# Optimization experiments

Measured on AMD Instinct MI355X. Metric: run time of the kernel, lower is better.

The kernel has to match this reference:

```python
import jax, jax.numpy as jnp
import numpy as np

# Sizes (see init_kwargs / shape_source)
N = 65536      # total points
B = 8          # batch elements
PPB = N // B   # points per batch element (8192, divisible by WS -> no padding)
D = 256        # d_model
H = 8          # nhead
DH = D // H
L = 4          # num_layers
FF = 2048      # torch TransformerEncoderLayer default dim_feedforward
RES = 128      # resolution (coordinate range / embedding table size)
BITS = 7       # ceil(log2(RES)); higher bits of morton loop are zero
WS = 128       # window_size
EPS = 1e-5     # LayerNorm eps


def setup_inputs() -> dict:
    key = jax.random.key(0)
    ks = jax.random.split(key, 16)
    s = 0.02
    batch_col = (jnp.arange(N) // PPB).astype(jnp.int32)
    xyz = jax.random.randint(ks[0], (N, 3), 0, RES, dtype=jnp.int32)
    coords = jnp.concatenate([batch_col[:, None], xyz], axis=1)
    features = jax.random.normal(ks[1], (N, D), jnp.float32)
    inp = {
        'coords': coords,
        'features': features,
        # learned positional embedding tables
        'pe_x': jax.random.normal(ks[2], (RES, D), jnp.float32) * s,
        'pe_y': jax.random.normal(ks[3], (RES, D), jnp.float32) * s,
        'pe_z': jax.random.normal(ks[4], (RES, D), jnp.float32) * s,
        'pe_s': jax.random.normal(ks[5], (RES, D), jnp.float32) * s,
        # stacked transformer encoder layer params (torch post-norm layer)
        'Wqkv': jax.random.normal(ks[6], (L, 3 * D, D), jnp.float32) * s,
        'bqkv': jnp.zeros((L, 3 * D), jnp.float32),
        'Wo': jax.random.normal(ks[7], (L, D, D), jnp.float32) * s,
        'bo': jnp.zeros((L, D), jnp.float32),
        'W1': jax.random.normal(ks[8], (L, FF, D), jnp.float32) * s,
        'b1': jnp.zeros((L, FF), jnp.float32),
        'W2': jax.random.normal(ks[9], (L, D, FF), jnp.float32) * s,
        'b2': jnp.zeros((L, D), jnp.float32),
        'g1': jnp.ones((L, D), jnp.float32),
        'be1': jnp.zeros((L, D), jnp.float32),
        'g2': jnp.ones((L, D), jnp.float32),
        'be2': jnp.zeros((L, D), jnp.float32),
    }
    return inp


def _morton_key(coords):
    # interleave bits of x,y,z (z lowest), prefix with batch index so batch order is preserved
    x, y, z = coords[:, 1], coords[:, 2], coords[:, 3]
    m = jnp.zeros_like(x)
    for i in range(BITS):
        m = m | (((x >> i) & 1) << (3 * i + 2)) \
              | (((y >> i) & 1) << (3 * i + 1)) \
              | (((z >> i) & 1) << (3 * i))
    return coords[:, 0] * (1 << (3 * BITS)) + m


def _ln(x, g, b):
    mu = jnp.mean(x, axis=-1, keepdims=True)
    var = jnp.mean(jnp.square(x - mu), axis=-1, keepdims=True)
    return (x - mu) * jax.lax.rsqrt(var + EPS) * g + b


def _encoder(x, params):
    # x: [Wn, WS, D]; torch TransformerEncoderLayer, post-norm, relu, no dropout (eval)
    scale = float(DH) ** -0.5

    def layer(h, p):
        Wqkv, bqkv, Wo, bo, W1, b1, W2, b2, g1, be1, g2, be2 = p
        Wn = h.shape[0]
        qkv = h @ Wqkv.T + bqkv                      # [Wn, WS, 3D]
        q, k, v = jnp.split(qkv, 3, axis=-1)
        q = q.reshape(Wn, WS, H, DH)
        k = k.reshape(Wn, WS, H, DH)
        v = v.reshape(Wn, WS, H, DH)
        att = jax.nn.softmax(jnp.einsum('wqhd,wkhd->whqk', q, k) * scale, axis=-1)
        o = jnp.einsum('whqk,wkhd->wqhd', att, v).reshape(Wn, WS, D) @ Wo.T + bo
        h = _ln(h + o, g1, be1)
        ff = jax.nn.relu(h @ W1.T + b1) @ W2.T + b2
        h = _ln(h + ff, g2, be2)
        return h, None

    x, _ = jax.lax.scan(layer, x, params)
    return x


def reference(coords, features, pe_x, pe_y, pe_z, pe_s,
              Wqkv, bqkv, Wo, bo, W1, b1, W2, b2, g1, be1, g2, be2):
    # 1) Morton sort (stable, batch-major)
    idx = jnp.argsort(_morton_key(coords))
    sc = coords[idx]
    sf = features[idx]
    # 2) learned positional encoding (stride = 1)
    pe = pe_x[sc[:, 1]] + pe_y[sc[:, 2]] + pe_z[sc[:, 3]] + pe_s[1]
    x = sf + pe
    # 3) window split: PPB % WS == 0, interval == 1 -> exact tiling, no padding
    x = x.reshape(-1, WS, D)                          # [Wn, WS, D]
    # 4) transformer encoder over windows
    x = _encoder(x, (Wqkv, bqkv, Wo, bo, W1, b1, W2, b2, g1, be1, g2, be2))
    # 5) gather back (all masks True -> simple reshape); output in sorted order
    return x.reshape(N, D)
```

## Files before the change

### kernel.cpp

```cpp
#include <hip/hip_runtime.h>

typedef unsigned int u32;
typedef unsigned short u16;

#define NPTS 65536
#define DMODEL 256
#define NHEAD 8
#define DHEAD 32
#define NLAYER 4
#define FFDIM 2048
#define WSIZE 128
#define LNEPS 1e-5f
#define RG 256

#define KSTR 36
#define VSTR 132
#define PSTR 132

typedef __attribute__((ext_vector_type(8))) short short8;
typedef __attribute__((ext_vector_type(4))) float floatx4;

__device__ __forceinline__ float bf2f(u16 v) {
    u32 u = ((u32)v) << 16;
    float f;
    __builtin_memcpy(&f, &u, 4);
    return f;
}
__device__ __forceinline__ u16 f2bf(float f) {
    u32 u;
    __builtin_memcpy(&u, &f, 4);
    u32 r = (u + 0x7fffu + ((u >> 16) & 1u)) >> 16;
    return (u16)r;
}

__device__ __forceinline__ void gl_lds16(const void* g, void* l) {
    __builtin_amdgcn_global_load_lds((const __attribute__((address_space(1))) u32*)g,
                                     (__attribute__((address_space(3))) u32*)l, 16, 0, 0);
}

__global__ __launch_bounds__(256) void morton_kernel(const int* __restrict__ coords,
                                                     u32* __restrict__ key, u32* __restrict__ val) {
    int i = blockIdx.x * 256 + threadIdx.x;
    int b = coords[4 * i + 0];
    int x = coords[4 * i + 1];
    int y = coords[4 * i + 2];
    int z = coords[4 * i + 3];
    u32 m = 0;
#pragma unroll
    for (int t = 0; t < 7; ++t) {
        m |= ((u32)((x >> t) & 1) << (3 * t + 2)) | ((u32)((y >> t) & 1) << (3 * t + 1)) |
             ((u32)((z >> t) & 1) << (3 * t));
    }
    key[i] = ((u32)b << 21) | m;
    val[i] = (u32)i;
}

__global__ __launch_bounds__(256) void hist_kernel(const u32* __restrict__ key, u32* __restrict__ ghist,
                                                   int shift) {
    __shared__ u32 h[256];
    int tid = threadIdx.x;
    h[tid] = 0;
    __syncthreads();
    u32 k = key[blockIdx.x * 256 + tid];
    atomicAdd(&h[(k >> shift) & 255u], 1u);
    __syncthreads();
    ghist[(size_t)tid * RG + blockIdx.x] = h[tid];
}

__global__ __launch_bounds__(256) void scan_up(u32* __restrict__ g, u32* __restrict__ aux) {
    __shared__ u32 wsum[4];
    int tid = threadIdx.x;
    int lane = tid & 63;
    int wave = tid >> 6;
    size_t base = (size_t)blockIdx.x * 1024 + (size_t)tid * 4;
    uint4 v = *(const uint4*)(g + base);
    u32 s = v.x + v.y + v.z + v.w;
    u32 inc = s;
#pragma unroll
    for (int off = 1; off < 64; off <<= 1) {
        u32 u = __shfl_up(inc, off, 64);
        if (lane >= off) inc += u;
    }
    if (lane == 63) wsum[wave] = inc;
    __syncthreads();
    u32 woff = 0;
    for (int w = 0; w < wave; ++w) woff += wsum[w];
    u32 excl = woff + inc - s;
    uint4 o;
    o.x = excl;
    o.y = excl + v.x;
    o.z = excl + v.x + v.y;
    o.w = excl + v.x + v.y + v.z;
    *(uint4*)(g + base) = o;
    if (tid == 255) aux[blockIdx.x] = woff + inc;
}

__global__ __launch_bounds__(256) void scan_down(u32* __restrict__ g, const u32* __restrict__ aux) {
    __shared__ u32 boff;
    int tid = threadIdx.x;
    if (tid < 64) {
        u32 a = (tid < (int)blockIdx.x) ? aux[tid] : 0u;
#pragma unroll
        for (int off = 32; off > 0; off >>= 1) a += __shfl_xor(a, off, 64);
        if (tid == 0) boff = a;
    }
    __syncthreads();
    u32 s = boff;
    size_t base = (size_t)blockIdx.x * 1024 + (size_t)tid * 4;
    uint4 v = *(uint4*)(g + base);
    v.x += s;
    v.y += s;
    v.z += s;
    v.w += s;
    *(uint4*)(g + base) = v;
}

__global__ __launch_bounds__(256) void scatter_kernel(const u32* __restrict__ keyin, const u32* __restrict__ valin,
                                                      u32* __restrict__ keyout, u32* __restrict__ valout,
                                                      const u32* __restrict__ ghist, int shift) {
    __shared__ u32 whist[4][256];
    int tid = threadIdx.x;
    int lane = tid & 63;
    int wave = tid >> 6;
    uint4 z = {0u, 0u, 0u, 0u};
    ((uint4*)&whist[0][0])[tid] = z;
    int gi = blockIdx.x * 256 + tid;
    u32 k = keyin[gi];
    u32 v = valin[gi];
    u32 b = (k >> shift) & 255u;
    __syncthreads();
    unsigned long long m = ~0ull;
#pragma unroll
    for (int bit = 0; bit < 8; ++bit) {
        unsigned long long bb = __ballot((int)((b >> bit) & 1u));
        m &= ((b >> bit) & 1u) ? bb : ~bb;
    }
    unsigned long long below = (lane == 0) ? 0ull : (m & ((1ull << lane) - 1ull));
    int rlane = __popcll(below);
    int cnt = __popcll(m);
    if (rlane == 0) whist[wave][b] = (u32)cnt;
    __syncthreads();
    u32 rank = (u32)rlane;
    for (int w = 0; w < wave; ++w) rank += whist[w][b];
    u32 dst = ghist[(size_t)b * RG + blockIdx.x] + rank;
    keyout[dst] = k;
    valout[dst] = v;
}

__global__ __launch_bounds__(256) void cvt_bf16_kernel(const float* __restrict__ in, u16* __restrict__ out, int n) {
    int i = blockIdx.x * 256 + threadIdx.x;
    if (i < n) out[i] = f2bf(in[i]);
}

template <bool HF32>
__global__ __launch_bounds__(256) void gather_pe_kernel(const u32* __restrict__ idx, const int* __restrict__ coords,
                                                        const float* __restrict__ feat,
                                                        const float* __restrict__ pex, const float* __restrict__ pey,
                                                        const float* __restrict__ pez, const float* __restrict__ pes,
                                                        float* __restrict__ h, u16* __restrict__ xb) {
    int row = blockIdx.x * 4 + (threadIdx.x >> 6);
    int lane = threadIdx.x & 63;
    int src = (int)idx[row];
    int cx = coords[4 * src + 1];
    int cy = coords[4 * src + 2];
    int cz = coords[4 * src + 3];
    int c = lane * 4;
    float4 f = *(const float4*)(feat + (size_t)src * DMODEL + c);
    float4 px = *(const float4*)(pex + (size_t)cx * DMODEL + c);
    float4 py = *(const float4*)(pey + (size_t)cy * DMODEL + c);
    float4 pz = *(const float4*)(pez + (size_t)cz * DMODEL + c);
    float4 ps = *(const float4*)(pes + (size_t)1 * DMODEL + c);
    float4 r;
    r.x = f.x + px.x + py.x + pz.x + ps.x;
    r.y = f.y + px.y + py.y + pz.y + ps.y;
    r.z = f.z + px.z + py.z + pz.z + ps.z;
    r.w = f.w + px.w + py.w + pz.w + ps.w;
    if (HF32) *(float4*)(h + (size_t)row * DMODEL + c) = r;
    ushort4 o;
    o.x = f2bf(r.x);
    o.y = f2bf(r.y);
    o.z = f2bf(r.z);
    o.w = f2bf(r.w);
    *(ushort4*)(xb + (size_t)row * DMODEL + c) = o;
}

template <bool RELU, bool BF16OUT>
__global__ __launch_bounds__(256) void gemm_bt(const u16* __restrict__ A, const u16* __restrict__ W,
                                               const float* __restrict__ bias, void* __restrict__ Cout,
                                               int M, int O, int K) {
    __shared__ __align__(16) u16 lA[128 * 64];
    __shared__ __align__(16) u16 lB[128 * 64];
    const int tid = threadIdx.x;
    const int lane = tid & 63;
    const int wave = tid >> 6;
    const int wr = wave >> 1;
    const int wc = wave & 1;
    const int quad = lane >> 4;
    const int l16 = lane & 15;
    const size_t row0 = (size_t)blockIdx.x * 128;
    const size_t col0 = (size_t)blockIdx.y * 128;
    floatx4 acc[4][4] = {};
    const u16* Abase = A + row0 * (size_t)K;
    const u16* Wbase = W + col0 * (size_t)K;

    for (int k0 = 0; k0 < K; k0 += 64) {
        __syncthreads();
#pragma unroll
        for (int it = 0; it < 4; ++it) {
            int cidx = tid + it * 256;
            int r = cidx >> 3;
            int cc = (cidx & 7) << 3;
            gl_lds16(Abase + (size_t)r * K + k0 + cc, &lA[cidx * 8]);
            gl_lds16(Wbase + (size_t)r * K + k0 + cc, &lB[cidx * 8]);
        }
        __syncthreads();
#pragma unroll
        for (int kk = 0; kk < 64; kk += 32) {
            short8 af[4], bf[4];
#pragma unroll
            for (int r = 0; r < 4; ++r)
                af[r] = *(const short8*)&lA[(wr * 64 + r * 16 + l16) * 64 + kk + quad * 8];
#pragma unroll
            for (int c = 0; c < 4; ++c)
                bf[c] = *(const short8*)&lB[(wc * 64 + c * 16 + l16) * 64 + kk + quad * 8];
#pragma unroll
            for (int r = 0; r < 4; ++r)
#pragma unroll
                for (int c = 0; c < 4; ++c)
                    acc[r][c] = __builtin_amdgcn_mfma_f32_16x16x32_bf16(af[r], bf[c], acc[r][c], 0, 0, 0);
        }
    }

#pragma unroll
    for (int r = 0; r < 4; ++r) {
#pragma unroll
        for (int c = 0; c < 4; ++c) {
            size_t col = col0 + wc * 64 + c * 16 + l16;
            float bv = bias[col];
#pragma unroll
            for (int reg = 0; reg < 4; ++reg) {
                size_t row = row0 + wr * 64 + r * 16 + quad * 4 + reg;
                float v = acc[r][c][reg] + bv;
                if (RELU) v = fmaxf(v, 0.f);
                if (BF16OUT)
                    ((u16*)Cout)[row * O + col] = f2bf(v);
                else
                    ((float*)Cout)[row * O + col] = v;
            }
        }
    }
}

__global__ __launch_bounds__(128) void attn_kernel(const u16* __restrict__ qkv, u16* __restrict__ outb) {
    const int wh = blockIdx.x;
    const int w = wh >> 3;
    const int h = wh & 7;
    const int tid = threadIdx.x;
    const int wave = tid >> 6;
    const int lane = tid & 63;
    const int quad = lane >> 4;
    const int l16 = lane & 15;
    __shared__ __align__(16) u16 lK[128 * KSTR];
    __shared__ __align__(16) u16 lVt[32 * VSTR];
    __shared__ __align__(16) u16 lP[128 * PSTR];
    const u16* base = qkv + (size_t)w * WSIZE * (3 * DMODEL);

    {
        const u16* krow = base + (size_t)tid * (3 * DMODEL) + DMODEL + h * DHEAD;
        const u16* vrow = base + (size_t)tid * (3 * DMODEL) + 2 * DMODEL + h * DHEAD;
#pragma unroll
        for (int p = 0; p < 4; ++p)
            *(short8*)&lK[tid * KSTR + p * 8] = *(const short8*)(krow + p * 8);
        u16 varr[32];
#pragma unroll
        for (int p = 0; p < 4; ++p)
            *(short8*)&varr[p * 8] = *(const short8*)(vrow + p * 8);
#pragma unroll
        for (int d = 0; d < DHEAD; ++d) lVt[d * VSTR + tid] = varr[d];
    }
    short8 af[4];
#pragma unroll
    for (int mi = 0; mi < 4; ++mi)
        af[mi] = *(const short8*)(base + (size_t)(wave * 64 + mi * 16 + l16) * (3 * DMODEL) + h * DHEAD + quad * 8);
    __syncthreads();

    floatx4 acc[4][8] = {};
#pragma unroll
    for (int ni = 0; ni < 8; ++ni) {
        short8 bk = *(const short8*)&lK[(ni * 16 + l16) * KSTR + quad * 8];
#pragma unroll
        for (int mi = 0; mi < 4; ++mi)
            acc[mi][ni] = __builtin_amdgcn_mfma_f32_16x16x32_bf16(af[mi], bk, acc[mi][ni], 0, 0, 0);
    }

    const float scale = 0.17677669529663687f;
    float inv[4][4];
#pragma unroll
    for (int mi = 0; mi < 4; ++mi) {
#pragma unroll
        for (int reg = 0; reg < 4; ++reg) {
            float m = acc[mi][0][reg];
#pragma unroll
            for (int ni = 1; ni < 8; ++ni) m = fmaxf(m, acc[mi][ni][reg]);
            m = fmaxf(m, __shfl_xor(m, 1, 64));
            m = fmaxf(m, __shfl_xor(m, 2, 64));
            m = fmaxf(m, __shfl_xor(m, 4, 64));
            m = fmaxf(m, __shfl_xor(m, 8, 64));
            float e[8];
            float sum = 0.f;
#pragma unroll
            for (int ni = 0; ni < 8; ++ni) {
                e[ni] = __expf((acc[mi][ni][reg] - m) * scale);
                sum += e[ni];
            }
            sum += __shfl_xor(sum, 1, 64);
            sum += __shfl_xor(sum, 2, 64);
            sum += __shfl_xor(sum, 4, 64);
            sum += __shfl_xor(sum, 8, 64);
            inv[mi][reg] = 1.f / sum;
            int row = wave * 64 + mi * 16 + quad * 4 + reg;
#pragma unroll
            for (int ni = 0; ni < 8; ++ni) lP[row * PSTR + ni * 16 + l16] = f2bf(e[ni]);
        }
    }

    floatx4 acc2[4][2] = {};
#pragma unroll
    for (int kt = 0; kt < 4; ++kt) {
        short8 pa[4];
#pragma unroll
        for (int mi = 0; mi < 4; ++mi)
            pa[mi] = *(const short8*)&lP[(wave * 64 + mi * 16 + l16) * PSTR + kt * 32 + quad * 8];
#pragma unroll
        for (int c = 0; c < 2; ++c) {
            short8 bv = *(const short8*)&lVt[(c * 16 + l16) * VSTR + kt * 32 + quad * 8];
#pragma unroll
            for (int mi = 0; mi < 4; ++mi)
                acc2[mi][c] = __builtin_amdgcn_mfma_f32_16x16x32_bf16(pa[mi], bv, acc2[mi][c], 0, 0, 0);
        }
    }

#pragma unroll
    for (int mi = 0; mi < 4; ++mi) {
#pragma unroll
        for (int c = 0; c < 2; ++c) {
#pragma unroll
            for (int reg = 0; reg < 4; ++reg) {
                int row = wave * 64 + mi * 16 + quad * 4 + reg;
                outb[(size_t)(w * WSIZE + row) * DMODEL + h * DHEAD + c * 16 + l16] =
                    f2bf(acc2[mi][c][reg] * inv[mi][reg]);
            }
        }
    }
}

template <bool HF32, bool OUTF32>
__global__ __launch_bounds__(256) void resid_ln_kernel(const void* __restrict__ hin, const float* __restrict__ delta,
                                                       const float* __restrict__ g, const float* __restrict__ b,
                                                       float* __restrict__ hout, void* __restrict__ nout) {
    int row = blockIdx.x * 4 + (threadIdx.x >> 6);
    int lane = threadIdx.x & 63;
    int c = lane * 4;
    float4 x;
    if (HF32) {
        x = *(const float4*)((const float*)hin + (size_t)row * DMODEL + c);
    } else {
        ushort4 hv = *(const ushort4*)((const u16*)hin + (size_t)row * DMODEL + c);
        x.x = bf2f(hv.x);
        x.y = bf2f(hv.y);
        x.z = bf2f(hv.z);
        x.w = bf2f(hv.w);
    }
    float4 d = *(const float4*)(delta + (size_t)row * DMODEL + c);
    x.x += d.x;
    x.y += d.y;
    x.z += d.z;
    x.w += d.w;
    float s = x.x + x.y + x.z + x.w;
#pragma unroll
    for (int off = 32; off > 0; off >>= 1) s += __shfl_xor(s, off, 64);
    float mu = s * (1.f / 256.f);
    float d0 = x.x - mu, d1 = x.y - mu, d2 = x.z - mu, d3 = x.w - mu;
    float vs = d0 * d0 + d1 * d1 + d2 * d2 + d3 * d3;
#pragma unroll
    for (int off = 32; off > 0; off >>= 1) vs += __shfl_xor(vs, off, 64);
    float rs = rsqrtf(vs * (1.f / 256.f) + LNEPS);
    float4 gg = *(const float4*)(g + c);
    float4 bb = *(const float4*)(b + c);
    float4 y;
    y.x = d0 * rs * gg.x + bb.x;
    y.y = d1 * rs * gg.y + bb.y;
    y.z = d2 * rs * gg.z + bb.z;
    y.w = d3 * rs * gg.w + bb.w;
    if (HF32) *(float4*)(hout + (size_t)row * DMODEL + c) = y;
    if (OUTF32) {
        *(float4*)((float*)nout + (size_t)row * DMODEL + c) = y;
    } else {
        ushort4 o;
        o.x = f2bf(y.x);
        o.y = f2bf(y.y);
        o.z = f2bf(y.z);
        o.w = f2bf(y.w);
        *(ushort4*)((u16*)nout + (size_t)row * DMODEL + c) = o;
    }
}

extern "C" void kernel_launch(void* const* d_in, const int* in_sizes, int n_in,
                              void* d_out, int out_size, void* d_ws, size_t ws_size,
                              hipStream_t stream) {
    (void)in_sizes;
    (void)n_in;
    (void)out_size;
    const int* coords = (const int*)d_in[0];
    const float* feat = (const float*)d_in[1];
    const float* pex = (const float*)d_in[2];
    const float* pey = (const float*)d_in[3];
    const float* pez = (const float*)d_in[4];
    const float* pes = (const float*)d_in[5];
    const float* Wqkv = (const float*)d_in[6];
    const float* bqkv = (const float*)d_in[7];
    const float* Wo = (const float*)d_in[8];
    const float* bo = (const float*)d_in[9];
    const float* W1 = (const float*)d_in[10];
    const float* b1 = (const float*)d_in[11];
    const float* W2 = (const float*)d_in[12];
    const float* b2 = (const float*)d_in[13];
    const float* g1 = (const float*)d_in[14];
    const float* be1 = (const float*)d_in[15];
    const float* g2 = (const float*)d_in[16];
    const float* be2 = (const float*)d_in[17];

    auto al = [](size_t x) { return (x + 255) & ~(size_t)255; };
    const size_t sortB = 4 * al((size_t)NPTS * 4) + al((size_t)256 * RG * 4) + 256;
    const size_t wqkvB = al((size_t)NLAYER * 3 * DMODEL * DMODEL * 2);
    const size_t woB = al((size_t)NLAYER * DMODEL * DMODEL * 2);
    const size_t w1B = al((size_t)NLAYER * FFDIM * DMODEL * 2);
    const size_t w2B = al((size_t)NLAYER * DMODEL * FFDIM * 2);
    const size_t wB = wqkvB + woB + w1B + w2B;
    const size_t xbB = al((size_t)NPTS * DMODEL * 2);
    const size_t hB = al((size_t)NPTS * DMODEL * 4);

    int CH = 0;
    bool modeA = true;
    for (int ch = 16384; ch >= 128; ch >>= 1) {
        size_t need = sortB + wB + xbB + hB + al((size_t)ch * 4096) + al((size_t)ch * 1024) + 65536;
        if (need <= ws_size) { CH = ch; modeA = true; break; }
    }
    if (!CH) {
        for (int ch = 16384; ch >= 128; ch >>= 1) {
            size_t need = sortB + wB + xbB + al((size_t)ch * 4096) + al((size_t)ch * 1024) + 65536;
            if (need <= ws_size) { CH = ch; modeA = false; break; }
        }
    }
    if (!CH) { CH = 128; modeA = false; }

    char* ws = (char*)d_ws;
    size_t off = 0;
    auto alloc = [&](size_t bytes) -> void* {
        void* p = ws + off;
        off += al(bytes);
        return p;
    };
    u32* key0 = (u32*)alloc(NPTS * 4);
    u32* val0 = (u32*)alloc(NPTS * 4);
    u32* key1 = (u32*)alloc(NPTS * 4);
    u32* val1 = (u32*)alloc(NPTS * 4);
    u32* ghist = (u32*)alloc(256 * RG * 4);
    u32* aux = (u32*)alloc(64 * 4);
    u16* wqkv_b = (u16*)alloc((size_t)NLAYER * 3 * DMODEL * DMODEL * 2);
    u16* wo_b = (u16*)alloc((size_t)NLAYER * DMODEL * DMODEL * 2);
    u16* w1_b = (u16*)alloc((size_t)NLAYER * FFDIM * DMODEL * 2);
    u16* w2_b = (u16*)alloc((size_t)NLAYER * DMODEL * FFDIM * 2);
    u16* xb = (u16*)alloc((size_t)NPTS * DMODEL * 2);
    float* h = modeA ? (float*)alloc((size_t)NPTS * DMODEL * 4) : nullptr;
    u16* scratch1 = (u16*)alloc((size_t)CH * 4096);
    float* tmpc = (float*)alloc((size_t)CH * 1024);

    morton_kernel<<<NPTS / 256, 256, 0, stream>>>(coords, key0, val0);

    u32 *ki = key0, *vi = val0, *ko = key1, *vo = val1;
    for (int p = 0; p < 3; ++p) {
        hist_kernel<<<RG, 256, 0, stream>>>(ki, ghist, p * 8);
        scan_up<<<64, 256, 0, stream>>>(ghist, aux);
        scan_down<<<64, 256, 0, stream>>>(ghist, aux);
        scatter_kernel<<<RG, 256, 0, stream>>>(ki, vi, ko, vo, ghist, p * 8);
        u32* t;
        t = ki; ki = ko; ko = t;
        t = vi; vi = vo; vo = t;
    }
    const u32* idx = vi;

    cvt_bf16_kernel<<<(NLAYER * 3 * DMODEL * DMODEL) / 256, 256, 0, stream>>>(Wqkv, wqkv_b, NLAYER * 3 * DMODEL * DMODEL);
    cvt_bf16_kernel<<<(NLAYER * DMODEL * DMODEL) / 256, 256, 0, stream>>>(Wo, wo_b, NLAYER * DMODEL * DMODEL);
    cvt_bf16_kernel<<<(NLAYER * FFDIM * DMODEL) / 256, 256, 0, stream>>>(W1, w1_b, NLAYER * FFDIM * DMODEL);
    cvt_bf16_kernel<<<(NLAYER * DMODEL * FFDIM) / 256, 256, 0, stream>>>(W2, w2_b, NLAYER * DMODEL * FFDIM);

    if (modeA)
        gather_pe_kernel<true><<<NPTS / 4, 256, 0, stream>>>(idx, coords, feat, pex, pey, pez, pes, h, xb);
    else
        gather_pe_kernel<false><<<NPTS / 4, 256, 0, stream>>>(idx, coords, feat, pex, pey, pez, pes, nullptr, xb);

    const int nch = NPTS / CH;
    u16* qkvc = scratch1;
    u16* attoutc = scratch1 + (size_t)CH * 768;
    u16* midc = scratch1;
    for (int l = 0; l < NLAYER; ++l) {
        for (int c = 0; c < nch; ++c) {
            u16* xc = xb + (size_t)c * CH * DMODEL;
            float* hc = modeA ? h + (size_t)c * CH * DMODEL : nullptr;
            gemm_bt<false, true><<<dim3(CH / 128, (3 * DMODEL) / 128), 256, 0, stream>>>(
                xc, wqkv_b + (size_t)l * 3 * DMODEL * DMODEL, bqkv + (size_t)l * 3 * DMODEL, qkvc,
                CH, 3 * DMODEL, DMODEL);
            attn_kernel<<<(CH / WSIZE) * NHEAD, 128, 0, stream>>>(qkvc, attoutc);
            gemm_bt<false, false><<<dim3(CH / 128, DMODEL / 128), 256, 0, stream>>>(
                attoutc, wo_b + (size_t)l * DMODEL * DMODEL, bo + (size_t)l * DMODEL, tmpc,
                CH, DMODEL, DMODEL);
            if (modeA)
                resid_ln_kernel<true, false><<<CH / 4, 256, 0, stream>>>(hc, tmpc, g1 + (size_t)l * DMODEL,
                                                                         be1 + (size_t)l * DMODEL, hc, xc);
            else
                resid_ln_kernel<false, false><<<CH / 4, 256, 0, stream>>>(xc, tmpc, g1 + (size_t)l * DMODEL,
                                                                          be1 + (size_t)l * DMODEL, nullptr, xc);
            gemm_bt<true, true><<<dim3(CH / 128, FFDIM / 128), 256, 0, stream>>>(
                xc, w1_b + (size_t)l * FFDIM * DMODEL, b1 + (size_t)l * FFDIM, midc,
                CH, FFDIM, DMODEL);
            gemm_bt<false, false><<<dim3(CH / 128, DMODEL / 128), 256, 0, stream>>>(
                midc, w2_b + (size_t)l * DMODEL * FFDIM, b2 + (size_t)l * DMODEL, tmpc,
                CH, DMODEL, FFDIM);
            bool last = (l == NLAYER - 1);
            void* outc = last ? (void*)((float*)d_out + (size_t)c * CH * DMODEL) : (void*)xc;
            if (modeA) {
                if (last)
                    resid_ln_kernel<true, true><<<CH / 4, 256, 0, stream>>>(hc, tmpc, g2 + (size_t)l * DMODEL,
                                                                            be2 + (size_t)l * DMODEL, hc, outc);
                else
                    resid_ln_kernel<true, false><<<CH / 4, 256, 0, stream>>>(hc, tmpc, g2 + (size_t)l * DMODEL,
                                                                             be2 + (size_t)l * DMODEL, hc, outc);
            } else {
                if (last)
                    resid_ln_kernel<false, true><<<CH / 4, 256, 0, stream>>>(xc, tmpc, g2 + (size_t)l * DMODEL,
                                                                             be2 + (size_t)l * DMODEL, nullptr, outc);
                else
                    resid_ln_kernel<false, false><<<CH / 4, 256, 0, stream>>>(xc, tmpc, g2 + (size_t)l * DMODEL,
                                                                              be2 + (size_t)l * DMODEL, nullptr, outc);
            }
        }
    }
}
```

Measured before the change: 2.662 ms.

## Double-buffer GEMM LDS tiles and allow larger FFN chunk sizes

The GEMM kernel now keeps two LDS buffers and issues the global-to-LDS loads for the next K tile before computing on the current one. It waits only on the older loads with a partial vmcnt and uses raw barriers, so memory latency can overlap with MFMA work. The chunk-size search for the FFN workspace now starts at the full point count, so fewer, larger chunks can be launched when workspace allows. The cost is double the LDS per block, which may lower occupancy, and the hand-written waitcnt count must match the loads actually issued.

After: 2.634 ms. About the same (-1.0%).

```diff
diff --git a/kernel.cpp b/kernel.cpp
--- a/kernel.cpp
+++ b/kernel.cpp
@@ -184,12 +184,24 @@
     *(ushort4*)(xb + (size_t)row * DMODEL + c) = o;
 }
 
+__device__ __forceinline__ void stage_tiles(const u16* __restrict__ Abase, const u16* __restrict__ Wbase,
+                                            int K, int k0, u16* la, u16* lb, int tid) {
+#pragma unroll
+    for (int it = 0; it < 4; ++it) {
+        int cidx = tid + it * 256;
+        int r = cidx >> 3;
+        int cc = (cidx & 7) << 3;
+        gl_lds16(Abase + (size_t)r * K + k0 + cc, la + cidx * 8);
+        gl_lds16(Wbase + (size_t)r * K + k0 + cc, lb + cidx * 8);
+    }
+}
+
 template <bool RELU, bool BF16OUT>
 __global__ __launch_bounds__(256) void gemm_bt(const u16* __restrict__ A, const u16* __restrict__ W,
                                                const float* __restrict__ bias, void* __restrict__ Cout,
                                                int M, int O, int K) {
-    __shared__ __align__(16) u16 lA[128 * 64];
-    __shared__ __align__(16) u16 lB[128 * 64];
+    __shared__ __align__(16) u16 lA[2][128 * 64];
+    __shared__ __align__(16) u16 lB[2][128 * 64];
     const int tid = threadIdx.x;
     const int lane = tid & 63;
     const int wave = tid >> 6;
@@ -203,32 +215,36 @@
     const u16* Abase = A + row0 * (size_t)K;
     const u16* Wbase = W + col0 * (size_t)K;
 
-    for (int k0 = 0; k0 < K; k0 += 64) {
-        __syncthreads();
-#pragma unroll
-        for (int it = 0; it < 4; ++it) {
-            int cidx = tid + it * 256;
-            int r = cidx >> 3;
-            int cc = (cidx & 7) << 3;
-            gl_lds16(Abase + (size_t)r * K + k0 + cc, &lA[cidx * 8]);
-            gl_lds16(Wbase + (size_t)r * K + k0 + cc, &lB[cidx * 8]);
-        }
-        __syncthreads();
+    const int nt = K >> 6;
+    stage_tiles(Abase, Wbase, K, 0, &lA[0][0], &lB[0][0], tid);
+    int buf = 0;
+    for (int t = 0; t < nt; ++t) {
+        if (t + 1 < nt) {
+            stage_tiles(Abase, Wbase, K, (t + 1) << 6, &lA[buf ^ 1][0], &lB[buf ^ 1][0], tid);
+            asm volatile("s_waitcnt vmcnt(8)" ::: "memory");
+        } else {
+            asm volatile("s_waitcnt vmcnt(0)" ::: "memory");
+        }
+        __builtin_amdgcn_s_barrier();
+        const u16* la = &lA[buf][0];
+        const u16* lb = &lB[buf][0];
 #pragma unroll
         for (int kk = 0; kk < 64; kk += 32) {
             short8 af[4], bf[4];
 #pragma unroll
             for (int r = 0; r < 4; ++r)
-                af[r] = *(const short8*)&lA[(wr * 64 + r * 16 + l16) * 64 + kk + quad * 8];
+                af[r] = *(const short8*)&la[(wr * 64 + r * 16 + l16) * 64 + kk + quad * 8];
 #pragma unroll
             for (int c = 0; c < 4; ++c)
-                bf[c] = *(const short8*)&lB[(wc * 64 + c * 16 + l16) * 64 + kk + quad * 8];
+                bf[c] = *(const short8*)&lb[(wc * 64 + c * 16 + l16) * 64 + kk + quad * 8];
 #pragma unroll
             for (int r = 0; r < 4; ++r)
 #pragma unroll
                 for (int c = 0; c < 4; ++c)
                     acc[r][c] = __builtin_amdgcn_mfma_f32_16x16x32_bf16(af[r], bf[c], acc[r][c], 0, 0, 0);
         }
+        if (t + 1 < nt) __builtin_amdgcn_s_barrier();
+        buf ^= 1;
     }
 
 #pragma unroll
@@ -442,12 +458,12 @@
 
     int CH = 0;
     bool modeA = true;
-    for (int ch = 16384; ch >= 128; ch >>= 1) {
+    for (int ch = 65536; ch >= 128; ch >>= 1) {
         size_t need = sortB + wB + xbB + hB + al((size_t)ch * 4096) + al((size_t)ch * 1024) + 65536;
         if (need <= ws_size) { CH = ch; modeA = true; break; }
     }
     if (!CH) {
-        for (int ch = 16384; ch >= 128; ch >>= 1) {
+        for (int ch = 65536; ch >= 128; ch >>= 1) {
             size_t need = sortB + wB + xbB + al((size_t)ch * 4096) + al((size_t)ch * 1024) + 65536;
             if (need <= ws_size) { CH = ch; modeA = false; break; }
         }
```
